# Optimization experiments

Hardware: AMD Instinct MI355X
Metric: run time of the kernel (lower is better)

The kernel has to match this reference:

```python
import jax, jax.numpy as jnp
import numpy as np

N_ATOMS = 5000
N_EDGES = 100000
F = 128          # num_features
B = 20           # num_basis (sinc expansion)
L = 3            # num_interactions
CUTOFF = 5.0
NUM_EMB = 119


def setup_inputs() -> dict:
    key = jax.random.key(0)
    ks = jax.random.split(key, 16)
    Z = jax.random.randint(ks[0], (N_ATOMS,), 1, NUM_EMB)
    edge_idx = jax.random.randint(ks[1], (N_EDGES, 2), 0, N_ATOMS)
    edge_dist = jax.random.uniform(ks[2], (N_EDGES,), minval=0.5, maxval=6.0, dtype=jnp.float32)
    u = jax.random.normal(ks[3], (N_EDGES, 3), dtype=jnp.float32)
    u = u / jnp.linalg.norm(u, axis=-1, keepdims=True)
    edge_diff = u * edge_dist[:, None]  # displacement vectors with |d| == edge_dist
    s = lambda k, shape: (jax.random.normal(k, shape, dtype=jnp.float32) * 0.05)
    inp = dict(Z=Z, edge_idx=edge_idx, edge_diff=edge_diff, edge_dist=edge_dist)
    inp.update(
        emb=s(ks[4], (NUM_EMB, F)),
        msg_w1=s(ks[5], (L, F, F)), msg_b1=jnp.zeros((L, F), jnp.float32),
        msg_w2=s(ks[6], (L, F, 3 * F)), msg_b2=jnp.zeros((L, 3 * F), jnp.float32),
        filt_w=s(ks[7], (L, B, 3 * F)), filt_b=jnp.zeros((L, 3 * F), jnp.float32),
        upd_U=s(ks[8], (L, F, F)), upd_V=s(ks[9], (L, F, F)),
        upd_w1=s(ks[10], (L, 2 * F, F)), upd_b1=jnp.zeros((L, F), jnp.float32),
        upd_w2=s(ks[11], (L, F, 3 * F)), upd_b2=jnp.zeros((L, 3 * F), jnp.float32),
        ro_w1=s(ks[12], (F, F // 2)), ro_b1=jnp.zeros((F // 2,), jnp.float32),
        ro_w2=s(ks[13], (F // 2, 1)), ro_b2=jnp.zeros((1,), jnp.float32),
    )
    return inp


def _painn(Z, edge_idx, edge_diff, edge_dist,
           emb, msg_w1, msg_b1, msg_w2, msg_b2, filt_w, filt_b,
           upd_U, upd_V, upd_w1, upd_b1, upd_w2, upd_b2,
           ro_w1, ro_b1, ro_w2, ro_b2):
    dtype = edge_diff.dtype
    # edge mask (equivalent to boolean compaction: masked edges contribute 0)
    mask = (edge_dist < CUTOFF).astype(dtype)
    dst = edge_idx[:, 0]  # receiver (index_add target)
    src = edge_idx[:, 1]  # sender (gathered neighbor)
    # sinc radial expansion: sin(n*pi*r/rc)/r, n = 1..B
    n = jnp.arange(1, B + 1, dtype=dtype)
    rbf = jnp.sin(edge_dist[:, None] * n * (jnp.pi / CUTOFF)) / edge_dist[:, None]  # [E,B]
    # cosine cutoff envelope, zeroed outside cutoff
    fc = 0.5 * (jnp.cos(jnp.pi * edge_dist / CUTOFF) + 1.0)
    env = (fc * mask)[:, None]  # [E,1]
    unit = edge_diff / edge_dist[:, None]  # [E,3]

    s_feat = emb[Z]                                   # [N,F]
    v_feat = jnp.zeros((Z.shape[0], 3, F), dtype)     # [N,3,F]

    for l in range(L):
        # ---- PainnMessage ----
        filt = (rbf @ filt_w[l] + filt_b[l]) * env                           # [E,3F]
        phi = jax.nn.silu(s_feat @ msg_w1[l] + msg_b1[l]) @ msg_w2[l] + msg_b2[l]  # [N,3F]
        fo = filt * phi[src]                                                  # [E,3F]
        gsv, gev, ms = jnp.split(fo, 3, axis=-1)                              # each [E,F]
        mv = v_feat[src] * gsv[:, None, :] + gev[:, None, :] * unit[:, :, None]  # [E,3,F]
        s_feat = s_feat + jnp.zeros_like(s_feat).at[dst].add(ms)
        v_feat = v_feat + jnp.zeros_like(v_feat).at[dst].add(mv)
        # ---- PainnUpdate ----
        Uv = jnp.einsum('nif,fg->nig', v_feat, upd_U[l])   # [N,3,F]
        Vv = jnp.einsum('nif,fg->nig', v_feat, upd_V[l])   # [N,3,F]
        Vn = jnp.linalg.norm(Vv, axis=1)                   # [N,F]
        a = jax.nn.silu(jnp.concatenate([s_feat, Vn], axis=-1) @ upd_w1[l] + upd_b1[l]) @ upd_w2[l] + upd_b2[l]
        avv, asv, ass = jnp.split(a, 3, axis=-1)
        v_feat = v_feat + avv[:, None, :] * Uv
        s_feat = s_feat + asv * jnp.sum(Uv * Vv, axis=1) + ass

    # atomwise readout MLP -> per-atom energy
    atom_energy = (jax.nn.silu(s_feat @ ro_w1 + ro_b1) @ ro_w2 + ro_b2)[:, 0]  # [N]
    return atom_energy


def reference(Z, edge_idx, edge_diff, edge_dist,
              emb, msg_w1, msg_b1, msg_w2, msg_b2, filt_w, filt_b,
              upd_U, upd_V, upd_w1, upd_b1, upd_w2, upd_b2,
              ro_w1, ro_b1, ro_w2, ro_b2):
    return _painn(Z, edge_idx, edge_diff, edge_dist,
                  emb, msg_w1, msg_b1, msg_w2, msg_b2, filt_w, filt_b,
                  upd_U, upd_V, upd_w1, upd_b1, upd_w2, upd_b2,
                  ro_w1, ro_b1, ro_w2, ro_b2)
```

## Files before the change

### kernel.cpp

```cpp
#include <hip/hip_runtime.h>
#include <hip/hip_bf16.h>
#include <hip/hip_fp16.h>
#include <math.h>

#define N_ATOMS 5000
#define N_EDGES 100000
#define F 128
#define B 20
#define NL 3
#define CAP 64

constexpr float CUTOFF = 5.0f;
constexpr float PI_F = 3.14159265358979323846f;

typedef _Float16 f16x8 __attribute__((ext_vector_type(8)));
typedef _Float16 h2 __attribute__((ext_vector_type(2)));
typedef float f32x4 __attribute__((ext_vector_type(4)));

struct EMeta { int src; float env; float u0, u1, u2; int pad[3]; };
struct __align__(4) U3 { unsigned int x, y, z; };

__device__ __forceinline__ float silu_f(float x) { return x / (1.0f + __expf(-x)); }

#define PV_IDX(atom, t) (((size_t)(atom) * F + (t)) * 6)

#define NB_INIT 2500
#define NB_BUCK 391

struct TPlanT { const float* src; _Float16* dst; int R, C, pad, blk0, tpc; };
struct TPlansT { TPlanT p[22]; int n; };

__global__ __launch_bounds__(256) void prep_kernel(
    const int* __restrict__ Z, const float* __restrict__ emb,
    float* __restrict__ s, _Float16* __restrict__ s_h,
    _Float16* __restrict__ pv,
    const int* __restrict__ eidx, int* __restrict__ count, int* __restrict__ bucket,
    TPlansT P) {
    __shared__ float tile[32][33];
    int b = blockIdx.x, tid = threadIdx.x;
    if (b < NB_INIT) {
        int atom = b * 2 + (tid >> 7);
        int t = tid & 127;
        float val = emb[Z[atom] * F + t];
        s[(size_t)atom * F + t] = val;
        s_h[(size_t)atom * F + t] = (_Float16)val;
        unsigned int* pp = (unsigned int*)(pv + PV_IDX(atom, t));
        pp[1] = 0u; pp[2] = 0u;
        return;
    }
    if (b < NB_INIT + NB_BUCK) {
        int e = (b - NB_INIT) * 256 + tid;
        if (e < N_EDGES) {
            int dst = eidx[2 * e];
            int pos = atomicAdd(&count[dst], 1);
            if (pos < CAP) bucket[dst * CAP + pos] = e;
        }
        return;
    }
    int tb = b - (NB_INIT + NB_BUCK);
    int pi = 0;
#pragma unroll
    for (int i = 1; i < 22; ++i)
        if (i < P.n && tb >= P.p[i].blk0) pi = i;
    const float* src = P.p[pi].src;
    _Float16* dst = P.p[pi].dst;
    int R = P.p[pi].R, C = P.p[pi].C, pad = P.p[pi].pad;
    int tl = tb - P.p[pi].blk0;
    int tpc = P.p[pi].tpc;
    int tr0 = (tl / tpc) * 32, tc0 = (tl % tpc) * 32;
    int i = tid >> 5, j = tid & 31;
#pragma unroll
    for (int rr = 0; rr < 4; ++rr) {
        int r = tr0 + i + 8 * rr, c = tc0 + j;
        if (r < R && c < C) tile[i + 8 * rr][j] = src[(size_t)r * C + c];
    }
    __syncthreads();
#pragma unroll
    for (int rr = 0; rr < 4; ++rr) {
        int c = tc0 + i + 8 * rr, r = tr0 + j;
        if (c < C && r < R) dst[(size_t)c * pad + r] = (_Float16)tile[j][i + 8 * rr];
    }
}

#define NB_META 1250

__global__ __launch_bounds__(256) void meta_phi_kernel(
    const int* __restrict__ count, const int* __restrict__ bucket,
    const int* __restrict__ eidx, const float* __restrict__ ediff,
    const float* __restrict__ edist,
    EMeta* __restrict__ meta, _Float16* __restrict__ rbfh,
    const _Float16* __restrict__ s_h, const _Float16* __restrict__ w1T,
    const float* __restrict__ b1, const _Float16* __restrict__ w2T,
    const float* __restrict__ b2, _Float16* __restrict__ pv) {
    __shared__ __align__(16) _Float16 shA[16 * 136];
    __shared__ __align__(16) _Float16 shH[16 * 136];
    int b = blockIdx.x, tid = threadIdx.x;
    if (b < NB_META) {
        int slot = b * 256 + tid;
        int a = slot >> 6, i = slot & (CAP - 1);
        if (i >= count[a]) return;
        int e = bucket[slot];
        float d = edist[e];
        EMeta m;
        m.src = eidx[2 * e + 1];
        float theta = d * (PI_F / CUTOFF);
        float s1 = __sinf(theta), c1 = __cosf(theta);
        float fc = 0.5f * (c1 + 1.0f);
        m.env = (d < CUTOFF) ? fc : 0.0f;
        float inv = 1.0f / d;
        m.u0 = ediff[3 * e + 0] * inv;
        m.u1 = ediff[3 * e + 1] * inv;
        m.u2 = ediff[3 * e + 2] * inv;
        m.pad[0] = m.pad[1] = m.pad[2] = 0;
        meta[slot] = m;
        _Float16* rp = rbfh + (size_t)slot * 24;
        float twoc = 2.0f * c1;
        float skm2 = 0.0f, skm1 = s1;
        rp[0] = (_Float16)(s1 * inv);
#pragma unroll
        for (int k = 2; k <= B; ++k) {
            float sk = twoc * skm1 - skm2;
            skm2 = skm1; skm1 = sk;
            rp[k - 1] = (_Float16)(sk * inv);
        }
        rp[20] = (_Float16)m.u0;
        rp[21] = (_Float16)m.u1;
        rp[22] = (_Float16)m.u2;
        rp[23] = (_Float16)0.0f;
        return;
    }
    int r0 = (b - NB_META) * 16;
    {
        int r = tid >> 4, c8 = (tid & 15) * 8;
        int rg = r0 + r; if (rg >= N_ATOMS) rg = N_ATOMS - 1;
        *(f16x8*)(shA + r * 136 + c8) = *(const f16x8*)(s_h + (size_t)rg * F + c8);
    }
    __syncthreads();
    int lane = tid & 63, wv = tid >> 6;
    int col = lane & 15, quad = lane >> 4;
    for (int nt = wv; nt < 8; nt += 4) {
        int n = nt * 16 + col;
        f32x4 acc = {0.f, 0.f, 0.f, 0.f};
#pragma unroll
        for (int kt = 0; kt < 4; ++kt) {
            f16x8 afr = *(const f16x8*)(shA + col * 136 + kt * 32 + quad * 8);
            f16x8 bfr = *(const f16x8*)(w1T + (size_t)n * 128 + kt * 32 + quad * 8);
            acc = __builtin_amdgcn_mfma_f32_16x16x32_f16(afr, bfr, acc, 0, 0, 0);
        }
        float bb = b1[n];
#pragma unroll
        for (int r = 0; r < 4; ++r)
            shH[(quad * 4 + r) * 136 + n] = (_Float16)silu_f(acc[r] + bb);
    }
    __syncthreads();
    for (int nt = wv; nt < 24; nt += 4) {
        int n = nt * 16 + col;
        f32x4 acc = {0.f, 0.f, 0.f, 0.f};
#pragma unroll
        for (int kt = 0; kt < 4; ++kt) {
            f16x8 afr = *(const f16x8*)(shH + col * 136 + kt * 32 + quad * 8);
            f16x8 bfr = *(const f16x8*)(w2T + (size_t)n * 128 + kt * 32 + quad * 8);
            acc = __builtin_amdgcn_mfma_f32_16x16x32_f16(afr, bfr, acc, 0, 0, 0);
        }
        float bb = b2[n];
#pragma unroll
        for (int r = 0; r < 4; ++r) {
            int row = r0 + quad * 4 + r;
            if (row < N_ATOMS)
                pv[PV_IDX(row, n & 127) + (n >> 7)] = (_Float16)(acc[r] + bb);
        }
    }
}

__global__ __launch_bounds__(256) void agg_kernel(
    const int* __restrict__ count, const EMeta* __restrict__ meta,
    const _Float16* __restrict__ rbfh,
    const _Float16* __restrict__ fwT, const float* __restrict__ fb,
    const _Float16* __restrict__ pv_r,
    float* __restrict__ s,
    _Float16* __restrict__ vmid_h) {
    int a = blockIdx.x;
    int tid = threadIdx.x;
    int t = tid & 127, team = tid >> 7;

    float s_old = 0.f;
    U3 vq = {0u, 0u, 0u};
    if (team == 0) {
        s_old = s[(size_t)a * F + t];
        vq = *(const U3*)(pv_r + PV_IDX(a, t));
    }

    unsigned int frw0[10], frw1[10], frw2[10];
    {
        const unsigned int* p0 = (const unsigned int*)(fwT + (size_t)t * 24);
        const unsigned int* p1 = (const unsigned int*)(fwT + (size_t)(F + t) * 24);
        const unsigned int* p2 = (const unsigned int*)(fwT + (size_t)(2 * F + t) * 24);
#pragma unroll
        for (int j = 0; j < 10; ++j) { frw0[j] = p0[j]; frw1[j] = p1[j]; frw2[j] = p2[j]; }
    }
    float fb0 = fb[t], fb1 = fb[F + t], fb2 = fb[2 * F + t];

    __shared__ int sh_src[CAP];
    __shared__ float sh_env[CAP];
    __shared__ __align__(16) unsigned int sh_rbf[CAP * 12];
    __shared__ float sh_part[4][F];

    int n = count[a]; if (n > CAP) n = CAP;
    const size_t aC = (size_t)a * CAP;
    if (tid < n) {
        const uint2 mp = *(const uint2*)(meta + aC + tid);
        sh_src[tid] = (int)mp.x;
        sh_env[tid] = __builtin_bit_cast(float, mp.y);
    }
    const unsigned int* rbf32 = (const unsigned int*)rbfh;
    for (int task = tid; task < n * 12; task += 256) {
        int i = task / 12, w = task - i * 12;
        sh_rbf[i * 12 + w] = rbf32[(aC + i) * 12 + w];
    }
    __syncthreads();

    float accS = 0.f, accV0 = 0.f, accV1 = 0.f, accV2 = 0.f;
    int myCnt = (n > team) ? ((n - team + 1) >> 1) : 0;
    if (myCnt > 0) {
        U3 QA[4], QB[4];
        int ngrp = (myCnt + 3) >> 2;
        auto load_grp = [&](int gbase, U3 Q[4]) {
#pragma unroll
            for (int j = 0; j < 4; ++j) {
                int i = gbase + j;
                int ii = (i < myCnt) ? i : (myCnt - 1);
                int src = sh_src[team + 2 * ii];
                Q[j] = *(const U3*)(pv_r + PV_IDX(src, t));
            }
        };
        auto comp_grp = [&](int gbase, U3 Q[4]) {
#pragma unroll
            for (int j = 0; j < 4; ++j) {
                int i = gbase + j;
                if (i < myCnt) {
                    int ei = team + 2 * i;
                    const uint4* rq = (const uint4*)(sh_rbf + ei * 12);
                    uint4 qa = rq[0], qb = rq[1];
                    uint4 qc = rq[2];
                    unsigned int rr[10] = {qa.x, qa.y, qa.z, qa.w,
                                           qb.x, qb.y, qb.z, qb.w, qc.x, qc.y};
                    float f0 = fb0, f1 = fb1, f2 = fb2;
#pragma unroll
                    for (int p = 0; p < 10; ++p) {
                        h2 rb = __builtin_bit_cast(h2, rr[p]);
                        f0 = __builtin_amdgcn_fdot2(rb, __builtin_bit_cast(h2, frw0[p]), f0, false);
                        f1 = __builtin_amdgcn_fdot2(rb, __builtin_bit_cast(h2, frw1[p]), f1, false);
                        f2 = __builtin_amdgcn_fdot2(rb, __builtin_bit_cast(h2, frw2[p]), f2, false);
                    }
                    float env = sh_env[ei];
                    f0 *= env; f1 *= env; f2 *= env;
                    h2 u01 = __builtin_bit_cast(h2, qc.z);
                    h2 u2p = __builtin_bit_cast(h2, qc.w);
                    h2 q0 = __builtin_bit_cast(h2, Q[j].x);
                    h2 q1 = __builtin_bit_cast(h2, Q[j].y);
                    h2 q2 = __builtin_bit_cast(h2, Q[j].z);
                    accS += f2 * (float)q1[0];
                    float gsv = f0 * (float)q0[0];
                    float gev = f1 * (float)q0[1];
                    accV0 += (float)q1[1] * gsv + gev * (float)u01[0];
                    accV1 += (float)q2[0] * gsv + gev * (float)u01[1];
                    accV2 += (float)q2[1] * gsv + gev * (float)u2p[0];
                }
            }
        };
        load_grp(0, QA);
        for (int g = 0; g < ngrp; g += 2) {
            if (g + 1 < ngrp) load_grp((g + 1) * 4, QB);
            comp_grp(g * 4, QA);
            if (g + 1 < ngrp) {
                if (g + 2 < ngrp) load_grp((g + 2) * 4, QA);
                comp_grp((g + 1) * 4, QB);
            }
        }
    }

    if (team == 1) {
        sh_part[0][t] = accS; sh_part[1][t] = accV0;
        sh_part[2][t] = accV1; sh_part[3][t] = accV2;
    }
    __syncthreads();
    if (team == 0) {
        h2 v1h = __builtin_bit_cast(h2, vq.y);
        h2 v2h = __builtin_bit_cast(h2, vq.z);
        float sm = s_old + accS + sh_part[0][t];
        s[(size_t)a * F + t] = sm;
        float vm0 = (float)v1h[1] + accV0 + sh_part[1][t];
        float vm1 = (float)v2h[0] + accV1 + sh_part[2][t];
        float vm2 = (float)v2h[1] + accV2 + sh_part[3][t];
        vmid_h[(size_t)(a * 3 + 0) * F + t] = (_Float16)vm0;
        vmid_h[(size_t)(a * 3 + 1) * F + t] = (_Float16)vm1;
        vmid_h[(size_t)(a * 3 + 2) * F + t] = (_Float16)vm2;
    }
}

__global__ __launch_bounds__(512) void fused_update_kernel(
    const _Float16* __restrict__ vmid_h, const _Float16* __restrict__ uvT,
    const _Float16* __restrict__ w1T, const float* __restrict__ b1,
    const _Float16* __restrict__ w2T, const float* __restrict__ b2,
    float* __restrict__ s, _Float16* __restrict__ pv_w,
    const _Float16* __restrict__ nw1T, const float* __restrict__ nb1,
    const _Float16* __restrict__ nw2T, const float* __restrict__ nb2,
    int do_phi,
    const _Float16* __restrict__ roT16, const float* __restrict__ rb1,
    const float* __restrict__ ro_w2p, const float* __restrict__ rb2,
    float* __restrict__ out, int do_ro) {
    __shared__ __align__(16) _Float16 shA[48 * 136];
    __shared__ __align__(16) _Float16 shUV[48 * 264];
    __shared__ __align__(16) _Float16 shCat[16 * 264];
    __shared__ __align__(16) _Float16 shH[16 * 136];
    __shared__ __align__(16) _Float16 shAa[16 * 392];
    _Float16* shS = shA;
    float* shRO = (float*)shAa;
    int a0 = blockIdx.x * 16;
    int r0 = a0 * 3;
    int tid = threadIdx.x;
    for (int slot = tid; slot < 48 * 16; slot += 512) {
        int r = slot >> 4, c8 = (slot & 15) * 8;
        int rg = r0 + r; if (rg >= N_ATOMS * 3) rg = N_ATOMS * 3 - 1;
        *(f16x8*)(shA + r * 136 + c8) = *(const f16x8*)(vmid_h + (size_t)rg * F + c8);
    }
    __syncthreads();
    int lane = tid & 63, wv = tid >> 6;
    int col = lane & 15, quad = lane >> 4;

    for (int j = wv; j < 48; j += 8) {
        int mt = j >> 4, nt = j & 15;
        int n = nt * 16 + col;
        f32x4 acc = {0.f, 0.f, 0.f, 0.f};
#pragma unroll
        for (int kt = 0; kt < 4; ++kt) {
            f16x8 afr = *(const f16x8*)(shA + (mt * 16 + col) * 136 + kt * 32 + quad * 8);
            f16x8 bfr = *(const f16x8*)(uvT + (size_t)n * 128 + kt * 32 + quad * 8);
            acc = __builtin_amdgcn_mfma_f32_16x16x32_f16(afr, bfr, acc, 0, 0, 0);
        }
#pragma unroll
        for (int r = 0; r < 4; ++r)
            shUV[(mt * 16 + quad * 4 + r) * 264 + n] = (_Float16)acc[r];
    }
    __syncthreads();

    for (int p = tid; p < 2048; p += 512) {
        int ai = p >> 7, t = p & 127;
        int atom = a0 + ai;
        int ag = (atom < N_ATOMS) ? atom : N_ATOMS - 1;
        shCat[ai * 264 + t] = (_Float16)s[(size_t)ag * F + t];
        float x0 = (float)shUV[(ai * 3 + 0) * 264 + 128 + t];
        float x1 = (float)shUV[(ai * 3 + 1) * 264 + 128 + t];
        float x2 = (float)shUV[(ai * 3 + 2) * 264 + 128 + t];
        shCat[ai * 264 + 128 + t] = (_Float16)sqrtf(x0 * x0 + x1 * x1 + x2 * x2);
    }
    __syncthreads();

    for (int nt = wv; nt < 8; nt += 8) {
        int n = nt * 16 + col;
        f32x4 acc = {0.f, 0.f, 0.f, 0.f};
#pragma unroll
        for (int kt = 0; kt < 8; ++kt) {
            f16x8 afr = *(const f16x8*)(shCat + col * 264 + kt * 32 + quad * 8);
            f16x8 bfr = *(const f16x8*)(w1T + (size_t)n * 256 + kt * 32 + quad * 8);
            acc = __builtin_amdgcn_mfma_f32_16x16x32_f16(afr, bfr, acc, 0, 0, 0);
        }
        float bb = b1[n];
#pragma unroll
        for (int r = 0; r < 4; ++r)
            shH[(quad * 4 + r) * 136 + n] = (_Float16)silu_f(acc[r] + bb);
    }
    __syncthreads();

    for (int nt = wv; nt < 24; nt += 8) {
        int n = nt * 16 + col;
        f32x4 acc = {0.f, 0.f, 0.f, 0.f};
#pragma unroll
        for (int kt = 0; kt < 4; ++kt) {
            f16x8 afr = *(const f16x8*)(shH + col * 136 + kt * 32 + quad * 8);
            f16x8 bfr = *(const f16x8*)(w2T + (size_t)n * 128 + kt * 32 + quad * 8);
            acc = __builtin_amdgcn_mfma_f32_16x16x32_f16(afr, bfr, acc, 0, 0, 0);
        }
        float bb = b2[n];
#pragma unroll
        for (int r = 0; r < 4; ++r)
            shAa[(quad * 4 + r) * 392 + n] = (_Float16)(acc[r] + bb);
    }
    __syncthreads();

    for (int p = tid; p < 2048; p += 512) {
        int ai = p >> 7, t = p & 127;
        int atom = a0 + ai;
        if (atom >= N_ATOMS) { shS[ai * 136 + t] = (_Float16)0.0f; continue; }
        float avv = (float)shAa[ai * 392 + t];
        float asv = (float)shAa[ai * 392 + 128 + t];
        float ass = (float)shAa[ai * 392 + 256 + t];
        float dot = 0.f;
        _Float16* pvp = pv_w + PV_IDX(atom, t);
#pragma unroll
        for (int d = 0; d < 3; ++d) {
            float u = (float)shUV[(ai * 3 + d) * 264 + t];
            float w = (float)shUV[(ai * 3 + d) * 264 + 128 + t];
            dot += u * w;
            float base = (float)vmid_h[(size_t)(atom * 3 + d) * F + t];
            float nv = base + avv * u;
            pvp[3 + d] = (_Float16)nv;
        }
        float sn = s[(size_t)atom * F + t] + asv * dot + ass;
        s[(size_t)atom * F + t] = sn;
        shS[ai * 136 + t] = (_Float16)sn;
    }

    if (do_phi) {
        __syncthreads();
        for (int nt = wv; nt < 8; nt += 8) {
            int n = nt * 16 + col;
            f32x4 acc = {0.f, 0.f, 0.f, 0.f};
#pragma unroll
            for (int kt = 0; kt < 4; ++kt) {
                f16x8 afr = *(const f16x8*)(shS + col * 136 + kt * 32 + quad * 8);
                f16x8 bfr = *(const f16x8*)(nw1T + (size_t)n * 128 + kt * 32 + quad * 8);
                acc = __builtin_amdgcn_mfma_f32_16x16x32_f16(afr, bfr, acc, 0, 0, 0);
            }
            float bb = nb1[n];
#pragma unroll
            for (int r = 0; r < 4; ++r)
                shH[(quad * 4 + r) * 136 + n] = (_Float16)silu_f(acc[r] + bb);
        }
        __syncthreads();
        for (int nt = wv; nt < 24; nt += 8) {
            int n = nt * 16 + col;
            f32x4 acc = {0.f, 0.f, 0.f, 0.f};
#pragma unroll
            for (int kt = 0; kt < 4; ++kt) {
                f16x8 afr = *(const f16x8*)(shH + col * 136 + kt * 32 + quad * 8);
                f16x8 bfr = *(const f16x8*)(nw2T + (size_t)n * 128 + kt * 32 + quad * 8);
                acc = __builtin_amdgcn_mfma_f32_16x16x32_f16(afr, bfr, acc, 0, 0, 0);
            }
            float bb = nb2[n];
#pragma unroll
            for (int r = 0; r < 4; ++r) {
                int row = a0 + quad * 4 + r;
                if (row < N_ATOMS)
                    pv_w[PV_IDX(row, n & 127) + (n >> 7)] = (_Float16)(acc[r] + bb);
            }
        }
    }

    if (do_ro) {
        __syncthreads();
        if (wv < 4) {
            int n = wv * 16 + col;
            f32x4 acc = {0.f, 0.f, 0.f, 0.f};
#pragma unroll
            for (int kt = 0; kt < 4; ++kt) {
                f16x8 afr = *(const f16x8*)(shS + col * 136 + kt * 32 + quad * 8);
                f16x8 bfr = *(const f16x8*)(roT16 + (size_t)n * 128 + kt * 32 + quad * 8);
                acc = __builtin_amdgcn_mfma_f32_16x16x32_f16(afr, bfr, acc, 0, 0, 0);
            }
            float bb = rb1[n], w2n = ro_w2p[n];
#pragma unroll
            for (int r = 0; r < 4; ++r)
                shRO[(quad * 4 + r) * 68 + n] = silu_f(acc[r] + bb) * w2n;
        }
        __syncthreads();
        if (tid < 16) {
            int atom = a0 + tid;
            if (atom < N_ATOMS) {
                float sum = rb2[0];
#pragma unroll 8
                for (int k = 0; k < 64; ++k) sum += shRO[tid * 68 + k];
                out[atom] = sum;
            }
        }
    }
}

extern "C" void kernel_launch(void* const* d_in, const int* in_sizes, int n_in,
                              void* d_out, int out_size, void* d_ws, size_t ws_size,
                              hipStream_t stream) {
    const int*   Z      = (const int*)d_in[0];
    const int*   eidx   = (const int*)d_in[1];
    const float* ediff  = (const float*)d_in[2];
    const float* edist  = (const float*)d_in[3];
    const float* emb    = (const float*)d_in[4];
    const float* msg_w1 = (const float*)d_in[5];
    const float* msg_b1 = (const float*)d_in[6];
    const float* msg_w2 = (const float*)d_in[7];
    const float* msg_b2 = (const float*)d_in[8];
    const float* filt_w = (const float*)d_in[9];
    const float* filt_b = (const float*)d_in[10];
    const float* upd_U  = (const float*)d_in[11];
    const float* upd_V  = (const float*)d_in[12];
    const float* upd_w1 = (const float*)d_in[13];
    const float* upd_b1 = (const float*)d_in[14];
    const float* upd_w2 = (const float*)d_in[15];
    const float* upd_b2 = (const float*)d_in[16];
    const float* ro_w1  = (const float*)d_in[17];
    const float* ro_b1  = (const float*)d_in[18];
    const float* ro_w2  = (const float*)d_in[19];
    const float* ro_b2  = (const float*)d_in[20];
    float* out = (float*)d_out;

    float* ws = (float*)d_ws;
    float* s   = ws;
    int* count  = (int*)(s + N_ATOMS * F);
    int* bucket = count + N_ATOMS;
    EMeta* meta = (EMeta*)(bucket + N_ATOMS * CAP);
    _Float16* rbfh = (_Float16*)(meta + N_ATOMS * CAP);
    _Float16* s_h  = rbfh + (size_t)N_ATOMS * CAP * 24;
    _Float16* vmid_h = s_h + (size_t)N_ATOMS * F;
    _Float16* pvA  = vmid_h + (size_t)N_ATOMS * 3 * F;
    _Float16* pvB  = pvA + (size_t)N_ATOMS * F * 6;
    _Float16* wh   = pvB + (size_t)N_ATOMS * F * 6;

    const int HWL = 16384 + 49152 + 32768 + 32768 + 49152 + 384 * 24;
    _Float16* mw1T = wh;
    _Float16* mw2T = wh + 16384;
    _Float16* uvT  = wh + 65536;
    _Float16* uw1T = wh + 98304;
    _Float16* uw2T = wh + 131072;
    _Float16* fwTl = wh + 180224;
    _Float16* roT16 = wh + (size_t)NL * HWL;

    TPlansT P; int nb = 0, pi = 0;
    auto add = [&](const float* src, _Float16* dst, int R, int C, int pad) {
        int tr = (R + 31) / 32, tc = (C + 31) / 32;
        P.p[pi].src = src; P.p[pi].dst = dst;
        P.p[pi].R = R; P.p[pi].C = C; P.p[pi].pad = pad;
        P.p[pi].blk0 = nb; P.p[pi].tpc = tc;
        nb += tr * tc; ++pi;
    };
    for (int l = 0; l < NL; ++l) {
        add(msg_w1 + l * F * F,     mw1T + (size_t)l * HWL, F, F, F);
        add(msg_w2 + l * F * 3 * F, mw2T + (size_t)l * HWL, F, 3 * F, F);
        add(upd_U  + l * F * F,     uvT  + (size_t)l * HWL, F, F, F);
        add(upd_V  + l * F * F,     uvT  + (size_t)l * HWL + F * F, F, F, F);
        add(upd_w1 + l * 2 * F * F, uw1T + (size_t)l * HWL, 2 * F, F, 2 * F);
        add(upd_w2 + l * F * 3 * F, uw2T + (size_t)l * HWL, F, 3 * F, F);
        add(filt_w + l * B * 3 * F, fwTl + (size_t)l * HWL, B, 3 * F, 24);
    }
    add(ro_w1, roT16, F, 64, F);
    P.n = pi;

    (void)hipMemsetAsync(count, 0, N_ATOMS * sizeof(int), stream);

    prep_kernel<<<NB_INIT + NB_BUCK + nb, 256, 0, stream>>>(
        Z, emb, s, s_h, pvA, eidx, count, bucket, P);

    const int GB16 = (N_ATOMS + 15) / 16;
    meta_phi_kernel<<<NB_META + GB16, 256, 0, stream>>>(
        count, bucket, eidx, ediff, edist, meta, rbfh,
        s_h, mw1T, msg_b1, mw2T, msg_b2, pvA);

    _Float16* pr = pvA;
    _Float16* pw = pvB;
    for (int l = 0; l < NL; ++l) {
        int do_phi = (l + 1 < NL);
        int do_ro = (l == NL - 1);
        int ln = do_phi ? (l + 1) : l;
        agg_kernel<<<N_ATOMS, 256, 0, stream>>>(
            count, meta, rbfh,
            fwTl + (size_t)l * HWL, filt_b + l * 3 * F,
            pr, s, vmid_h);
        fused_update_kernel<<<GB16, 512, 0, stream>>>(
            vmid_h, uvT + (size_t)l * HWL,
            uw1T + (size_t)l * HWL, upd_b1 + l * F,
            uw2T + (size_t)l * HWL, upd_b2 + l * 3 * F,
            s, pw,
            mw1T + (size_t)ln * HWL, msg_b1 + ln * F,
            mw2T + (size_t)ln * HWL, msg_b2 + ln * 3 * F, do_phi,
            roT16, ro_b1, ro_w2, ro_b2, out, do_ro);
        _Float16* tmp = pr; pr = pw; pw = tmp;
    }
}
```

Before: 318.0 us.

## Fuse edge metadata and RBF computation into bucketing pass, shrink EMeta

Edge metadata (source index, envelope) and the sinc radial basis plus unit vectors are now computed directly in the prep kernel's bucketing pass, at the slot claimed by the atomic. This removes the intermediate bucket array and the second pass over it in the former meta_phi kernel, which becomes a pure phi kernel. EMeta shrinks from 32 to 8 bytes, since the unit vectors already live in the rbf buffer. The fused update kernel now reads the vmid base values from shared memory instead of global, and aliases shS to shCat so the vmid tile stays intact. The bucketing pass now carries more per-thread work and scattered writes behind the atomic.

```diff
diff --git a/kernel.cpp b/kernel.cpp
--- a/kernel.cpp
+++ b/kernel.cpp
@@ -17,7 +17,7 @@
 typedef _Float16 h2 __attribute__((ext_vector_type(2)));
 typedef float f32x4 __attribute__((ext_vector_type(4)));
 
-struct EMeta { int src; float env; float u0, u1, u2; int pad[3]; };
+struct EMeta { int src; float env; };
 struct __align__(4) U3 { unsigned int x, y, z; };
 
 __device__ __forceinline__ float silu_f(float x) { return x / (1.0f + __expf(-x)); }
@@ -34,7 +34,9 @@
     const int* __restrict__ Z, const float* __restrict__ emb,
     float* __restrict__ s, _Float16* __restrict__ s_h,
     _Float16* __restrict__ pv,
-    const int* __restrict__ eidx, int* __restrict__ count, int* __restrict__ bucket,
+    const int* __restrict__ eidx, const float* __restrict__ ediff,
+    const float* __restrict__ edist,
+    int* __restrict__ count, EMeta* __restrict__ meta, _Float16* __restrict__ rbfh,
     TPlansT P) {
     __shared__ float tile[32][33];
     int b = blockIdx.x, tid = threadIdx.x;
@@ -52,8 +54,32 @@
         int e = (b - NB_INIT) * 256 + tid;
         if (e < N_EDGES) {
             int dst = eidx[2 * e];
+            int srcA = eidx[2 * e + 1];
             int pos = atomicAdd(&count[dst], 1);
-            if (pos < CAP) bucket[dst * CAP + pos] = e;
+            if (pos < CAP) {
+                int slot = dst * CAP + pos;
+                float d = edist[e];
+                float theta = d * (PI_F / CUTOFF);
+                float s1 = __sinf(theta), c1 = __cosf(theta);
+                float env = (d < CUTOFF) ? 0.5f * (c1 + 1.0f) : 0.0f;
+                float inv = 1.0f / d;
+                EMeta mm; mm.src = srcA; mm.env = env;
+                meta[slot] = mm;
+                _Float16* rp = rbfh + (size_t)slot * 24;
+                float twoc = 2.0f * c1;
+                float skm2 = 0.0f, skm1 = s1;
+                rp[0] = (_Float16)(s1 * inv);
+#pragma unroll
+                for (int k = 2; k <= B; ++k) {
+                    float sk = twoc * skm1 - skm2;
+                    skm2 = skm1; skm1 = sk;
+                    rp[k - 1] = (_Float16)(sk * inv);
+                }
+                rp[20] = (_Float16)(ediff[3 * e + 0] * inv);
+                rp[21] = (_Float16)(ediff[3 * e + 1] * inv);
+                rp[22] = (_Float16)(ediff[3 * e + 2] * inv);
+                rp[23] = (_Float16)0.0f;
+            }
         }
         return;
     }
@@ -82,54 +108,14 @@
     }
 }
 
-#define NB_META 1250
-
-__global__ __launch_bounds__(256) void meta_phi_kernel(
-    const int* __restrict__ count, const int* __restrict__ bucket,
-    const int* __restrict__ eidx, const float* __restrict__ ediff,
-    const float* __restrict__ edist,
-    EMeta* __restrict__ meta, _Float16* __restrict__ rbfh,
+__global__ __launch_bounds__(256) void phi_kernel(
     const _Float16* __restrict__ s_h, const _Float16* __restrict__ w1T,
     const float* __restrict__ b1, const _Float16* __restrict__ w2T,
     const float* __restrict__ b2, _Float16* __restrict__ pv) {
     __shared__ __align__(16) _Float16 shA[16 * 136];
     __shared__ __align__(16) _Float16 shH[16 * 136];
-    int b = blockIdx.x, tid = threadIdx.x;
-    if (b < NB_META) {
-        int slot = b * 256 + tid;
-        int a = slot >> 6, i = slot & (CAP - 1);
-        if (i >= count[a]) return;
-        int e = bucket[slot];
-        float d = edist[e];
-        EMeta m;
-        m.src = eidx[2 * e + 1];
-        float theta = d * (PI_F / CUTOFF);
-        float s1 = __sinf(theta), c1 = __cosf(theta);
-        float fc = 0.5f * (c1 + 1.0f);
-        m.env = (d < CUTOFF) ? fc : 0.0f;
-        float inv = 1.0f / d;
-        m.u0 = ediff[3 * e + 0] * inv;
-        m.u1 = ediff[3 * e + 1] * inv;
-        m.u2 = ediff[3 * e + 2] * inv;
-        m.pad[0] = m.pad[1] = m.pad[2] = 0;
-        meta[slot] = m;
-        _Float16* rp = rbfh + (size_t)slot * 24;
-        float twoc = 2.0f * c1;
-        float skm2 = 0.0f, skm1 = s1;
-        rp[0] = (_Float16)(s1 * inv);
-#pragma unroll
-        for (int k = 2; k <= B; ++k) {
-            float sk = twoc * skm1 - skm2;
-            skm2 = skm1; skm1 = sk;
-            rp[k - 1] = (_Float16)(sk * inv);
-        }
-        rp[20] = (_Float16)m.u0;
-        rp[21] = (_Float16)m.u1;
-        rp[22] = (_Float16)m.u2;
-        rp[23] = (_Float16)0.0f;
-        return;
-    }
-    int r0 = (b - NB_META) * 16;
+    int r0 = blockIdx.x * 16;
+    int tid = threadIdx.x;
     {
         int r = tid >> 4, c8 = (tid & 15) * 8;
         int rg = r0 + r; if (rg >= N_ATOMS) rg = N_ATOMS - 1;
@@ -314,7 +300,7 @@
     __shared__ __align__(16) _Float16 shCat[16 * 264];
     __shared__ __align__(16) _Float16 shH[16 * 136];
     __shared__ __align__(16) _Float16 shAa[16 * 392];
-    _Float16* shS = shA;
+    _Float16* shS = shCat;
     float* shRO = (float*)shAa;
     int a0 = blockIdx.x * 16;
     int r0 = a0 * 3;
@@ -402,7 +388,7 @@
             float u = (float)shUV[(ai * 3 + d) * 264 + t];
             float w = (float)shUV[(ai * 3 + d) * 264 + 128 + t];
             dot += u * w;
-            float base = (float)vmid_h[(size_t)(atom * 3 + d) * F + t];
+            float base = (float)shA[(ai * 3 + d) * 136 + t];
             float nv = base + avv * u;
             pvp[3 + d] = (_Float16)nv;
         }
@@ -505,9 +491,8 @@
     float* ws = (float*)d_ws;
     float* s   = ws;
     int* count  = (int*)(s + N_ATOMS * F);
-    int* bucket = count + N_ATOMS;
-    EMeta* meta = (EMeta*)(bucket + N_ATOMS * CAP);
-    _Float16* rbfh = (_Float16*)(meta + N_ATOMS * CAP);
+    EMeta* meta = (EMeta*)(count + N_ATOMS);
+    _Float16* rbfh = (_Float16*)(meta + (size_t)N_ATOMS * CAP);
     _Float16* s_h  = rbfh + (size_t)N_ATOMS * CAP * 24;
     _Float16* vmid_h = s_h + (size_t)N_ATOMS * F;
     _Float16* pvA  = vmid_h + (size_t)N_ATOMS * 3 * F;
@@ -546,11 +531,10 @@
     (void)hipMemsetAsync(count, 0, N_ATOMS * sizeof(int), stream);
 
     prep_kernel<<<NB_INIT + NB_BUCK + nb, 256, 0, stream>>>(
-        Z, emb, s, s_h, pvA, eidx, count, bucket, P);
+        Z, emb, s, s_h, pvA, eidx, ediff, edist, count, meta, rbfh, P);
 
     const int GB16 = (N_ATOMS + 15) / 16;
-    meta_phi_kernel<<<NB_META + GB16, 256, 0, stream>>>(
-        count, bucket, eidx, ediff, edist, meta, rbfh,
+    phi_kernel<<<GB16, 256, 0, stream>>>(
         s_h, mw1T, msg_b1, mw2T, msg_b2, pvA);
 
     _Float16* pr = pvA;
```

After: 318.9 us. No clear change (+0.3%).
